# Performance work log

Measured on AMD Instinct MI355X. Metric: run time of the kernel, lower is better.

Reference implementation:

```python
import jax, jax.numpy as jnp
import numpy as np

DIM = 768
HEADS = 12
HEAD_DIM = DIM // HEADS
EPS = 1e-5


def setup_inputs() -> dict:
    key = jax.random.key(0)
    ks = jax.random.split(key, 9)
    s = 0.02
    x = jax.random.normal(ks[0], (4, 1024, DIM), dtype=jnp.float32)
    return {
        "x": x,
        "Wqkv_c": jax.random.normal(ks[1], (DIM, 3 * DIM), jnp.float32) * s,
        "bqkv_c": jnp.zeros((3 * DIM,), jnp.float32),
        "Wp_c": jax.random.normal(ks[2], (DIM, DIM), jnp.float32) * s,
        "bp_c": jnp.zeros((DIM,), jnp.float32),
        "Wqkv_ac": jax.random.normal(ks[3], (DIM, 3 * DIM), jnp.float32) * s,
        "bqkv_ac": jnp.zeros((3 * DIM,), jnp.float32),
        "Wp_ac": jax.random.normal(ks[4], (DIM, DIM), jnp.float32) * s,
        "bp_ac": jnp.zeros((DIM,), jnp.float32),
        "gamma": jnp.ones((DIM,), jnp.float32),
        "beta": jnp.zeros((DIM,), jnp.float32),
    }


def _branch(x, Wqkv, bqkv, Wp, bp, causal: bool):
    B, T, C = x.shape
    qkv = (x @ Wqkv + bqkv).reshape(B, T, 3, HEADS, HEAD_DIM)
    qkv = jnp.transpose(qkv, (2, 0, 3, 1, 4))  # [3,B,H,T,Dh]
    q, k, v = qkv[0], qkv[1], qkv[2]
    scores = jnp.einsum("bhqd,bhkd->bhqk", q, k) / np.sqrt(HEAD_DIM).astype(np.float32)
    i = jnp.arange(T)[:, None]
    j = jnp.arange(T)[None, :]
    mask = (j <= i) if causal else (j >= i)  # tril / triu (incl. diagonal)
    scores = jnp.where(mask[None, None], scores, -jnp.inf)
    attn = jax.nn.softmax(scores, axis=-1)
    out = jnp.einsum("bhqk,bhkd->bhqd", attn, v)
    out = jnp.transpose(out, (0, 2, 1, 3)).reshape(B, T, C)
    return out @ Wp + bp


def reference(x, Wqkv_c, bqkv_c, Wp_c, bp_c, Wqkv_ac, bqkv_ac, Wp_ac, bp_ac, gamma, beta):
    out_c = _branch(x, Wqkv_c, bqkv_c, Wp_c, bp_c, causal=True)
    out_ac = _branch(x, Wqkv_ac, bqkv_ac, Wp_ac, bp_ac, causal=False)
    y = x + out_c + out_ac  # residual; dropout is identity at eval
    mu = jnp.mean(y, axis=-1, keepdims=True)
    var = jnp.var(y, axis=-1, keepdims=True)
    return (y - mu) * jax.lax.rsqrt(var + EPS) * gamma + beta
```

## Files before the change

### kernel.cpp

```cpp
#include <hip/hip_runtime.h>
#include <stdint.h>

#define DIM 768
#define HEADS 12
#define HD 64
#define BATCH 4
#define SEQ 1024
#define NTOK (BATCH*SEQ)
#define QKVW (3*DIM)
#define QKW (2*DIM)
#define EPS 1e-5f

typedef __attribute__((ext_vector_type(8))) short short8;
typedef __attribute__((ext_vector_type(4))) float f32x4;

__device__ __forceinline__ unsigned short f2bf(float f) {
    union { float f; unsigned u; } v; v.f = f;
    unsigned r = v.u + 0x7fffu + ((v.u >> 16) & 1u);
    return (unsigned short)(r >> 16);
}

__device__ __forceinline__ void gld_lds16(const void* g, void* l) {
    auto gp = reinterpret_cast<const __attribute__((address_space(1))) unsigned int*>(
        (uintptr_t)g);
    auto lp = reinterpret_cast<__attribute__((address_space(3))) unsigned int*>(
        (unsigned int)(uintptr_t)l);
    __builtin_amdgcn_global_load_lds(gp, lp, 16, 0, 0);
}

__global__ __launch_bounds__(256) void cvt_kernel(
    const float* __restrict__ in, unsigned short* __restrict__ out)
{
    const int i = blockIdx.x * 256 + threadIdx.x;
    const float4 v = ((const float4*)in)[i];
    ushort4 o4;
    o4.x = f2bf(v.x); o4.y = f2bf(v.y); o4.z = f2bf(v.z); o4.w = f2bf(v.w);
    ((ushort4*)out)[i] = o4;
}

__global__ __launch_bounds__(256) void cvtT_kernel(
    const float* __restrict__ W0, const float* __restrict__ W1,
    unsigned short* __restrict__ T0, unsigned short* __restrict__ T1,
    const int K, const int N)
{
    const float* __restrict__ W = blockIdx.z ? W1 : W0;
    unsigned short* __restrict__ WT = blockIdx.z ? T1 : T0;
    __shared__ float t[32][33];
    const int n0 = blockIdx.x * 32, k0 = blockIdx.y * 32;
    const int c = threadIdx.x & 31, rr = threadIdx.x >> 5;
#pragma unroll
    for (int i = 0; i < 4; ++i)
        t[rr + 8 * i][c] = W[(size_t)(k0 + rr + 8 * i) * N + n0 + c];
    __syncthreads();
#pragma unroll
    for (int i = 0; i < 4; ++i)
        WT[(size_t)(n0 + rr + 8 * i) * K + k0 + c] = f2bf(t[c][rr + 8 * i]);
}

__global__ __launch_bounds__(256) void gemm_qkv_kernel(
    const unsigned short* __restrict__ A,
    const unsigned short* __restrict__ BT0, const unsigned short* __restrict__ BT1,
    const float* __restrict__ bias0, const float* __restrict__ bias1,
    unsigned short* __restrict__ QK0, unsigned short* __restrict__ QK1,
    unsigned short* __restrict__ VT0, unsigned short* __restrict__ VT1)
{
    const int z = blockIdx.z;
    const unsigned short* __restrict__ BT = z ? BT1 : BT0;
    const float* __restrict__ bias = z ? bias1 : bias0;
    unsigned short* __restrict__ QK = z ? QK1 : QK0;
    unsigned short* __restrict__ VT = z ? VT1 : VT0;
    const int K = DIM;

    __shared__ __align__(16) unsigned short Als[2][128 * 32];
    __shared__ __align__(16) unsigned short Bls[2][128 * 32];
    const int tid = threadIdx.x, lane = tid & 63, wv = tid >> 6;
    const int m0 = blockIdx.y * 128, n0 = blockIdx.x * 128;
    const int wr = wv >> 1, wc = wv & 1;
    const int fm = lane & 15, fk = (lane >> 4) * 8;
    const int c0 = wv * 2;
    const int arow = c0 * 16 + (lane >> 2), kk = (lane & 3) * 8;

    const unsigned short* Ag0 = A  + (size_t)(m0 + arow)      * K + kk;
    const unsigned short* Ag1 = A  + (size_t)(m0 + arow + 16) * K + kk;
    const unsigned short* Bg0 = BT + (size_t)(n0 + arow)      * K + kk;
    const unsigned short* Bg1 = BT + (size_t)(n0 + arow + 16) * K + kk;

    f32x4 acc[4][4];
#pragma unroll
    for (int i = 0; i < 4; ++i)
#pragma unroll
        for (int j = 0; j < 4; ++j) acc[i][j] = f32x4{0.f, 0.f, 0.f, 0.f};

    gld_lds16(Ag0, &Als[0][c0 * 512]);
    gld_lds16(Ag1, &Als[0][c0 * 512 + 512]);
    gld_lds16(Bg0, &Bls[0][c0 * 512]);
    gld_lds16(Bg1, &Bls[0][c0 * 512 + 512]);

    const int NK = K / 32;
    for (int kt = 0; kt < NK; ++kt) {
        const int p = kt & 1;
        __syncthreads();
        if (kt + 1 < NK) {
            const int off = (kt + 1) * 32;
            gld_lds16(Ag0 + off, &Als[p ^ 1][c0 * 512]);
            gld_lds16(Ag1 + off, &Als[p ^ 1][c0 * 512 + 512]);
            gld_lds16(Bg0 + off, &Bls[p ^ 1][c0 * 512]);
            gld_lds16(Bg1 + off, &Bls[p ^ 1][c0 * 512 + 512]);
        }
        short8 af[4], bf[4];
#pragma unroll
        for (int i = 0; i < 4; ++i)
            af[i] = *(const short8*)&Als[p][(wr * 64 + i * 16 + fm) * 32 + fk];
#pragma unroll
        for (int j = 0; j < 4; ++j)
            bf[j] = *(const short8*)&Bls[p][(wc * 64 + j * 16 + fm) * 32 + fk];
#pragma unroll
        for (int i = 0; i < 4; ++i)
#pragma unroll
            for (int j = 0; j < 4; ++j)
                acc[i][j] = __builtin_amdgcn_mfma_f32_16x16x32_bf16(af[i], bf[j], acc[i][j], 0, 0, 0);
    }
    const int rbase = (lane >> 4) * 4;
    if (n0 < QKW) {
        const float qsc = (n0 < DIM) ? 0.125f : 1.0f;
#pragma unroll
        for (int i = 0; i < 4; ++i) {
            const int m = m0 + wr * 64 + i * 16 + rbase;
#pragma unroll
            for (int j = 0; j < 4; ++j) {
                const int n = n0 + wc * 64 + j * 16 + fm;
                const float bs = bias[n];
#pragma unroll
                for (int r = 0; r < 4; ++r)
                    QK[(size_t)(m + r) * QKW + n] = f2bf((acc[i][j][r] + bs) * qsc);
            }
        }
    } else {
#pragma unroll
        for (int i = 0; i < 4; ++i) {
            const int m = m0 + wr * 64 + i * 16 + rbase;
            const int b = m >> 10, t = m & 1023;
#pragma unroll
            for (int j = 0; j < 4; ++j) {
                const int n = n0 + wc * 64 + j * 16 + fm;
                const int nh = n - QKW;
                const float bs = bias[n];
                const unsigned p0 = f2bf(acc[i][j][0] + bs);
                const unsigned p1 = f2bf(acc[i][j][1] + bs);
                const unsigned p2 = f2bf(acc[i][j][2] + bs);
                const unsigned p3 = f2bf(acc[i][j][3] + bs);
                uint2 u; u.x = p0 | (p1 << 16); u.y = p2 | (p3 << 16);
                *(uint2*)(VT + ((size_t)((b * HEADS + (nh >> 6)) * HD + (nh & 63)) * SEQ + t)) = u;
            }
        }
    }
}

__global__ __launch_bounds__(256) void gemm_proj_kernel(
    const unsigned short* __restrict__ A0, const unsigned short* __restrict__ BT0,
    const unsigned short* __restrict__ A1, const unsigned short* __restrict__ BT1,
    const float* __restrict__ b0, const float* __restrict__ b1,
    const float* __restrict__ xres, float* __restrict__ Y0, float* __restrict__ Y1)
{
    const int z = blockIdx.z;
    const unsigned short* __restrict__ A  = z ? A1 : A0;
    const unsigned short* __restrict__ BT = z ? BT1 : BT0;
    __shared__ __align__(16) unsigned short Als[2][64 * 32];
    __shared__ __align__(16) unsigned short Bls[2][128 * 32];
    const int tid = threadIdx.x, lane = tid & 63, wv = tid >> 6;
    const int m0 = blockIdx.y * 64, n0 = blockIdx.x * 128;
    const int fm = lane & 15, fg = lane >> 4, fk = (lane >> 4) * 8;
    const int srw = lane >> 2, kk = (lane & 3) * 8;
    const int K = DIM;

    const unsigned short* Ag  = A  + (size_t)(m0 + wv * 16 + srw) * K + kk;
    const unsigned short* Bg0 = BT + (size_t)(n0 + wv * 32 + srw) * K + kk;
    const unsigned short* Bg1 = BT + (size_t)(n0 + wv * 32 + 16 + srw) * K + kk;

    f32x4 acc[4][2];
#pragma unroll
    for (int i = 0; i < 4; ++i)
#pragma unroll
        for (int j = 0; j < 2; ++j) acc[i][j] = f32x4{0.f, 0.f, 0.f, 0.f};

    gld_lds16(Ag,  &Als[0][wv * 512]);
    gld_lds16(Bg0, &Bls[0][wv * 1024]);
    gld_lds16(Bg1, &Bls[0][wv * 1024 + 512]);

    const int NK = K / 32;
    for (int kt = 0; kt < NK; ++kt) {
        const int p = kt & 1;
        __syncthreads();
        if (kt + 1 < NK) {
            const int off = (kt + 1) * 32;
            gld_lds16(Ag + off,  &Als[p ^ 1][wv * 512]);
            gld_lds16(Bg0 + off, &Bls[p ^ 1][wv * 1024]);
            gld_lds16(Bg1 + off, &Bls[p ^ 1][wv * 1024 + 512]);
        }
        short8 af[4], bf[2];
#pragma unroll
        for (int i = 0; i < 4; ++i)
            af[i] = *(const short8*)&Als[p][(i * 16 + fm) * 32 + fk];
#pragma unroll
        for (int j = 0; j < 2; ++j)
            bf[j] = *(const short8*)&Bls[p][(wv * 32 + j * 16 + fm) * 32 + fk];
#pragma unroll
        for (int i = 0; i < 4; ++i)
#pragma unroll
            for (int j = 0; j < 2; ++j)
                acc[i][j] = __builtin_amdgcn_mfma_f32_16x16x32_bf16(af[i], bf[j], acc[i][j], 0, 0, 0);
    }
#pragma unroll
    for (int i = 0; i < 4; ++i) {
        const int m = m0 + i * 16 + fg * 4;
#pragma unroll
        for (int j = 0; j < 2; ++j) {
            const int n = n0 + wv * 32 + j * 16 + fm;
            if (z == 0) {
                const float bs = b0[n] + b1[n];
#pragma unroll
                for (int r = 0; r < 4; ++r) {
                    const size_t idx = (size_t)(m + r) * DIM + n;
                    Y0[idx] = acc[i][j][r] + xres[idx] + bs;
                }
            } else {
#pragma unroll
                for (int r = 0; r < 4; ++r)
                    Y1[(size_t)(m + r) * DIM + n] = acc[i][j][r];
            }
        }
    }
}

#define KP 72
__global__ __launch_bounds__(256, 3) void attn_fused_kernel(
    const unsigned short* __restrict__ qk_c, const unsigned short* __restrict__ vT_c,
    const unsigned short* __restrict__ qk_ac, const unsigned short* __restrict__ vT_ac,
    unsigned short* __restrict__ o_c, unsigned short* __restrict__ o_ac)
{
    __shared__ __align__(16) unsigned short Kls[2][64 * KP];
    __shared__ __align__(16) unsigned short Vls[2][64 * KP];
    __shared__ __align__(16) unsigned short Ps[4][16 * KP];
    const int tid = threadIdx.x, lane = tid & 63, w = tid >> 6;
    const int fm = lane & 15, fg = lane >> 4;
    const int bh = blockIdx.x, qt = blockIdx.y;
    const int b = bh / HEADS, h = bh % HEADS;
    unsigned short* Psw = &Ps[w][0];
    const int srow = tid >> 3, sseg = (tid & 7) * 8;

    for (int br = 0; br < 2; ++br) {
        const int causal = (br == 0);
        const unsigned short* __restrict__ qk = causal ? qk_c : qk_ac;
        const unsigned short* __restrict__ vT = causal ? vT_c : vT_ac;
        unsigned short* __restrict__ o = causal ? o_c : o_ac;
        const unsigned short* qbase = qk + (size_t)b * SEQ * QKW + h * HD;
        const unsigned short* kbase = qbase + DIM;
        const unsigned short* vtb   = vT + (size_t)(b * HEADS + h) * HD * SEQ;

        short8 qb0, qb1;
        {
            const size_t qoff = (size_t)(qt * 64 + w * 16 + fm) * QKW + fg * 8;
            qb0 = *(const short8*)(qbase + qoff);
            qb1 = *(const short8*)(qbase + qoff + 32);
        }

        float ls = 0.f;
        f32x4 accO[4];
#pragma unroll
        for (int dj = 0; dj < 4; ++dj) accO[dj] = f32x4{0.f, 0.f, 0.f, 0.f};

        const int ktb = causal ? 0 : qt;
        const int kte = causal ? qt : (SEQ / 64 - 1);

        uint4 kr0 = *(const uint4*)(kbase + (size_t)(ktb * 64 + srow) * QKW + sseg);
        uint4 kr1 = *(const uint4*)(kbase + (size_t)(ktb * 64 + srow + 32) * QKW + sseg);
        uint4 vr0 = *(const uint4*)(vtb + (size_t)srow * SEQ + ktb * 64 + sseg);
        uint4 vr1 = *(const uint4*)(vtb + (size_t)(srow + 32) * SEQ + ktb * 64 + sseg);

        if (br) __syncthreads();
        int p = 0;
        for (int kt = ktb; kt <= kte; ++kt) {
            *(uint4*)(&Kls[p][srow * KP + sseg])        = kr0;
            *(uint4*)(&Kls[p][(srow + 32) * KP + sseg]) = kr1;
            *(uint4*)(&Vls[p][srow * KP + sseg])        = vr0;
            *(uint4*)(&Vls[p][(srow + 32) * KP + sseg]) = vr1;
            if (kt < kte) {
                const int ktn = kt + 1;
                kr0 = *(const uint4*)(kbase + (size_t)(ktn * 64 + srow) * QKW + sseg);
                kr1 = *(const uint4*)(kbase + (size_t)(ktn * 64 + srow + 32) * QKW + sseg);
                vr0 = *(const uint4*)(vtb + (size_t)srow * SEQ + ktn * 64 + sseg);
                vr1 = *(const uint4*)(vtb + (size_t)(srow + 32) * SEQ + ktn * 64 + sseg);
            }
            __syncthreads();

            f32x4 st[4];
#pragma unroll
            for (int kj = 0; kj < 4; ++kj) {
                const short8 ka0 = *(const short8*)&Kls[p][(kj * 16 + fm) * KP + fg * 8];
                const short8 ka1 = *(const short8*)&Kls[p][(kj * 16 + fm) * KP + 32 + fg * 8];
                st[kj] = __builtin_amdgcn_mfma_f32_16x16x32_bf16(ka0, qb0, f32x4{0.f,0.f,0.f,0.f}, 0, 0, 0);
                st[kj] = __builtin_amdgcn_mfma_f32_16x16x32_bf16(ka1, qb1, st[kj], 0, 0, 0);
            }
            const bool diag = (kt == qt);
#pragma unroll
            for (int kj = 0; kj < 4; ++kj) {
                float e[4];
#pragma unroll
                for (int r = 0; r < 4; ++r) {
                    float v = st[kj][r];
                    if (diag) {
                        const int ki = kj * 16 + fg * 4 + r;
                        const int qi = w * 16 + fm;
                        const bool ok = causal ? (ki <= qi) : (ki >= qi);
                        if (!ok) v = -1e30f;
                    }
                    e[r] = __expf(v);
                    ls += e[r];
                }
                const unsigned p0 = f2bf(e[0]);
                const unsigned p1 = f2bf(e[1]);
                const unsigned p2 = f2bf(e[2]);
                const unsigned p3 = f2bf(e[3]);
                uint2 u; u.x = p0 | (p1 << 16); u.y = p2 | (p3 << 16);
                *(uint2*)(Psw + fm * KP + kj * 16 + fg * 4) = u;
            }
            const short8 ap0 = *(const short8*)(Psw + fm * KP + fg * 8);
            const short8 ap1 = *(const short8*)(Psw + fm * KP + 32 + fg * 8);
#pragma unroll
            for (int dj = 0; dj < 4; ++dj) {
                const short8 vb0 = *(const short8*)&Vls[p][(dj * 16 + fm) * KP + fg * 8];
                const short8 vb1 = *(const short8*)&Vls[p][(dj * 16 + fm) * KP + 32 + fg * 8];
                accO[dj] = __builtin_amdgcn_mfma_f32_16x16x32_bf16(ap0, vb0, accO[dj], 0, 0, 0);
                accO[dj] = __builtin_amdgcn_mfma_f32_16x16x32_bf16(ap1, vb1, accO[dj], 0, 0, 0);
            }
            p ^= 1;
        }

        float lt = ls;
        lt += __shfl_xor(lt, 16);
        lt += __shfl_xor(lt, 32);
        float li_o[4];
#pragma unroll
        for (int r = 0; r < 4; ++r) li_o[r] = __shfl(lt, fg * 4 + r);
#pragma unroll
        for (int r = 0; r < 4; ++r) {
            const float inv = 1.f / li_o[r];
            const int q = qt * 64 + w * 16 + fg * 4 + r;
            unsigned short* orow = o + ((size_t)b * SEQ + q) * DIM + h * HD;
#pragma unroll
            for (int dj = 0; dj < 4; ++dj)
                orow[dj * 16 + fm] = f2bf(accO[dj][r] * inv);
        }
    }
}

__global__ __launch_bounds__(256) void ln_kernel(
    const float* __restrict__ Y0, const float* __restrict__ Y1,
    const float* __restrict__ gamma, const float* __restrict__ beta,
    float* __restrict__ out)
{
    const int row = blockIdx.x;
    const int tid = threadIdx.x;
    const float* y0r = Y0 + (size_t)row * DIM;
    const float* y1r = Y1 + (size_t)row * DIM;
    float v0 = y0r[tid] + y1r[tid];
    float v1 = y0r[tid + 256] + y1r[tid + 256];
    float v2 = y0r[tid + 512] + y1r[tid + 512];
    float s = v0 + v1 + v2;
    float q = v0 * v0 + v1 * v1 + v2 * v2;
#pragma unroll
    for (int off = 32; off > 0; off >>= 1) {
        s += __shfl_down(s, off);
        q += __shfl_down(q, off);
    }
    __shared__ float rs_[4], rq_[4];
    const int wv = tid >> 6;
    if ((tid & 63) == 0) { rs_[wv] = s; rq_[wv] = q; }
    __syncthreads();
    const float ts = rs_[0] + rs_[1] + rs_[2] + rs_[3];
    const float tq = rq_[0] + rq_[1] + rq_[2] + rq_[3];
    const float mu = ts * (1.f / DIM);
    const float var = tq * (1.f / DIM) - mu * mu;
    const float rstd = rsqrtf(var + EPS);
    out[(size_t)row * DIM + tid]       = (v0 - mu) * rstd * gamma[tid]       + beta[tid];
    out[(size_t)row * DIM + tid + 256] = (v1 - mu) * rstd * gamma[tid + 256] + beta[tid + 256];
    out[(size_t)row * DIM + tid + 512] = (v2 - mu) * rstd * gamma[tid + 512] + beta[tid + 512];
}

extern "C" void kernel_launch(void* const* d_in, const int* in_sizes, int n_in,
                              void* d_out, int out_size, void* d_ws, size_t ws_size,
                              hipStream_t stream)
{
    const float* x       = (const float*)d_in[0];
    const float* Wqkv_c  = (const float*)d_in[1];
    const float* bqkv_c  = (const float*)d_in[2];
    const float* Wp_c    = (const float*)d_in[3];
    const float* bp_c    = (const float*)d_in[4];
    const float* Wqkv_ac = (const float*)d_in[5];
    const float* bqkv_ac = (const float*)d_in[6];
    const float* Wp_ac   = (const float*)d_in[7];
    const float* bp_ac   = (const float*)d_in[8];
    const float* gamma   = (const float*)d_in[9];
    const float* beta    = (const float*)d_in[10];
    float* out = (float*)d_out;

    char* p = (char*)d_ws;
    unsigned short* qk_c   = (unsigned short*)p; p += (size_t)NTOK * QKW * 2;
    unsigned short* qk_ac  = (unsigned short*)p; p += (size_t)NTOK * QKW * 2;
    unsigned short* vT_c   = (unsigned short*)p; p += (size_t)NTOK * DIM * 2;
    unsigned short* vT_ac  = (unsigned short*)p; p += (size_t)NTOK * DIM * 2;
    unsigned short* o_ac   = (unsigned short*)p; p += (size_t)NTOK * DIM * 2;
    unsigned short* xb     = (unsigned short*)p; p += (size_t)NTOK * DIM * 2;
    unsigned short* WqT_c  = (unsigned short*)p; p += (size_t)QKVW * DIM * 2;
    unsigned short* WqT_ac = (unsigned short*)p; p += (size_t)QKVW * DIM * 2;
    unsigned short* WpT_c  = (unsigned short*)p; p += (size_t)DIM * DIM * 2;
    unsigned short* WpT_ac = (unsigned short*)p; p += (size_t)DIM * DIM * 2;
    unsigned short* o_c = WqT_c;
    float*          Y0  = (float*)qk_c;
    float*          Y1  = (float*)vT_c;

    cvt_kernel<<<NTOK * DIM / 1024, 256, 0, stream>>>(x, xb);
    cvtT_kernel<<<dim3(QKVW / 32, DIM / 32, 2), 256, 0, stream>>>(
        Wqkv_c, Wqkv_ac, WqT_c, WqT_ac, DIM, QKVW);
    cvtT_kernel<<<dim3(DIM / 32, DIM / 32, 2), 256, 0, stream>>>(
        Wp_c, Wp_ac, WpT_c, WpT_ac, DIM, DIM);

    gemm_qkv_kernel<<<dim3(QKVW / 128, NTOK / 128, 2), 256, 0, stream>>>(
        xb, WqT_c, WqT_ac, bqkv_c, bqkv_ac, qk_c, qk_ac, vT_c, vT_ac);

    attn_fused_kernel<<<dim3(BATCH * HEADS, SEQ / 64), 256, 0, stream>>>(
        qk_c, vT_c, qk_ac, vT_ac, o_c, o_ac);

    gemm_proj_kernel<<<dim3(DIM / 128, NTOK / 64, 2), 256, 0, stream>>>(
        o_c, WpT_c, o_ac, WpT_ac, bp_c, bp_ac, x, Y0, Y1);
    ln_kernel<<<NTOK, 256, 0, stream>>>(Y0, Y1, gamma, beta, out);
}
```

Before: 205.1 us.

## Merge conversion kernels, stage QKV epilogue through LDS, store second projection in bf16

The three input and weight conversion kernels are merged into a single launch that picks its work from the block index. The QKV GEMM epilogue now stages results in a padded shared buffer and writes them out with coalesced 16-byte stores, for both the QK rows and the transposed V. The second projection output is stored as bf16 instead of fp32 to cut write and read traffic into the layernorm. That last step rounds one branch's projection output to bf16 before the residual sum and layernorm, which costs some precision.

Result: faster. 199.9 us (-2.5%).

```diff
diff --git a/kernel.cpp b/kernel.cpp
--- a/kernel.cpp
+++ b/kernel.cpp
@@ -19,6 +19,9 @@
     unsigned r = v.u + 0x7fffu + ((v.u >> 16) & 1u);
     return (unsigned short)(r >> 16);
 }
+__device__ __forceinline__ float b2f(unsigned short s) {
+    union { unsigned u; float f; } v; v.u = (unsigned)s << 16; return v.f;
+}
 
 __device__ __forceinline__ void gld_lds16(const void* g, void* l) {
     auto gp = reinterpret_cast<const __attribute__((address_space(1))) unsigned int*>(
@@ -28,26 +31,40 @@
     __builtin_amdgcn_global_load_lds(gp, lp, 16, 0, 0);
 }
 
-__global__ __launch_bounds__(256) void cvt_kernel(
-    const float* __restrict__ in, unsigned short* __restrict__ out)
-{
-    const int i = blockIdx.x * 256 + threadIdx.x;
-    const float4 v = ((const float4*)in)[i];
-    ushort4 o4;
-    o4.x = f2bf(v.x); o4.y = f2bf(v.y); o4.z = f2bf(v.z); o4.w = f2bf(v.w);
-    ((ushort4*)out)[i] = o4;
-}
-
-__global__ __launch_bounds__(256) void cvtT_kernel(
-    const float* __restrict__ W0, const float* __restrict__ W1,
-    unsigned short* __restrict__ T0, unsigned short* __restrict__ T1,
-    const int K, const int N)
-{
-    const float* __restrict__ W = blockIdx.z ? W1 : W0;
-    unsigned short* __restrict__ WT = blockIdx.z ? T1 : T0;
+#define CVT_X_BLOCKS (NTOK*DIM/1024)
+#define CVT_WQ_TILES ((QKVW/32)*(DIM/32))
+#define CVT_WP_TILES ((DIM/32)*(DIM/32))
+__global__ __launch_bounds__(256) void cvt_all_kernel(
+    const float* __restrict__ x,
+    const float* __restrict__ Wq0, const float* __restrict__ Wq1,
+    const float* __restrict__ Wp0, const float* __restrict__ Wp1,
+    unsigned short* __restrict__ xb,
+    unsigned short* __restrict__ WqT0, unsigned short* __restrict__ WqT1,
+    unsigned short* __restrict__ WpT0, unsigned short* __restrict__ WpT1)
+{
+    const int bid = blockIdx.x, tid = threadIdx.x;
+    if (bid < CVT_X_BLOCKS) {
+        const int i = bid * 256 + tid;
+        const float4 v = ((const float4*)x)[i];
+        ushort4 o4;
+        o4.x = f2bf(v.x); o4.y = f2bf(v.y); o4.z = f2bf(v.z); o4.w = f2bf(v.w);
+        ((ushort4*)xb)[i] = o4;
+        return;
+    }
     __shared__ float t[32][33];
-    const int n0 = blockIdx.x * 32, k0 = blockIdx.y * 32;
-    const int c = threadIdx.x & 31, rr = threadIdx.x >> 5;
+    const float* W; unsigned short* WT; int N, K, tile;
+    int w = bid - CVT_X_BLOCKS;
+    if (w < 2 * CVT_WQ_TILES) {
+        const int z = w / CVT_WQ_TILES; tile = w % CVT_WQ_TILES;
+        W = z ? Wq1 : Wq0; WT = z ? WqT1 : WqT0; N = QKVW; K = DIM;
+    } else {
+        w -= 2 * CVT_WQ_TILES;
+        const int z = w / CVT_WP_TILES; tile = w % CVT_WP_TILES;
+        W = z ? Wp1 : Wp0; WT = z ? WpT1 : WpT0; N = DIM; K = DIM;
+    }
+    const int ntiles = N / 32;
+    const int n0 = (tile % ntiles) * 32, k0 = (tile / ntiles) * 32;
+    const int c = tid & 31, rr = tid >> 5;
 #pragma unroll
     for (int i = 0; i < 4; ++i)
         t[rr + 8 * i][c] = W[(size_t)(k0 + rr + 8 * i) * N + n0 + c];
@@ -71,8 +88,7 @@
     unsigned short* __restrict__ VT = z ? VT1 : VT0;
     const int K = DIM;
 
-    __shared__ __align__(16) unsigned short Als[2][128 * 32];
-    __shared__ __align__(16) unsigned short Bls[2][128 * 32];
+    __shared__ __align__(16) unsigned short sh[17408];
     const int tid = threadIdx.x, lane = tid & 63, wv = tid >> 6;
     const int m0 = blockIdx.y * 128, n0 = blockIdx.x * 128;
     const int wr = wv >> 1, wc = wv & 1;
@@ -91,10 +107,10 @@
 #pragma unroll
         for (int j = 0; j < 4; ++j) acc[i][j] = f32x4{0.f, 0.f, 0.f, 0.f};
 
-    gld_lds16(Ag0, &Als[0][c0 * 512]);
-    gld_lds16(Ag1, &Als[0][c0 * 512 + 512]);
-    gld_lds16(Bg0, &Bls[0][c0 * 512]);
-    gld_lds16(Bg1, &Bls[0][c0 * 512 + 512]);
+    gld_lds16(Ag0, &sh[c0 * 512]);
+    gld_lds16(Ag1, &sh[c0 * 512 + 512]);
+    gld_lds16(Bg0, &sh[4096 + c0 * 512]);
+    gld_lds16(Bg1, &sh[4096 + c0 * 512 + 512]);
 
     const int NK = K / 32;
     for (int kt = 0; kt < NK; ++kt) {
@@ -102,56 +118,76 @@
         __syncthreads();
         if (kt + 1 < NK) {
             const int off = (kt + 1) * 32;
-            gld_lds16(Ag0 + off, &Als[p ^ 1][c0 * 512]);
-            gld_lds16(Ag1 + off, &Als[p ^ 1][c0 * 512 + 512]);
-            gld_lds16(Bg0 + off, &Bls[p ^ 1][c0 * 512]);
-            gld_lds16(Bg1 + off, &Bls[p ^ 1][c0 * 512 + 512]);
-        }
+            const int q = (p ^ 1) * 8192;
+            gld_lds16(Ag0 + off, &sh[q + c0 * 512]);
+            gld_lds16(Ag1 + off, &sh[q + c0 * 512 + 512]);
+            gld_lds16(Bg0 + off, &sh[q + 4096 + c0 * 512]);
+            gld_lds16(Bg1 + off, &sh[q + 4096 + c0 * 512 + 512]);
+        }
+        const int pb = p * 8192;
         short8 af[4], bf[4];
 #pragma unroll
         for (int i = 0; i < 4; ++i)
-            af[i] = *(const short8*)&Als[p][(wr * 64 + i * 16 + fm) * 32 + fk];
+            af[i] = *(const short8*)&sh[pb + (wr * 64 + i * 16 + fm) * 32 + fk];
 #pragma unroll
         for (int j = 0; j < 4; ++j)
-            bf[j] = *(const short8*)&Bls[p][(wc * 64 + j * 16 + fm) * 32 + fk];
+            bf[j] = *(const short8*)&sh[pb + 4096 + (wc * 64 + j * 16 + fm) * 32 + fk];
 #pragma unroll
         for (int i = 0; i < 4; ++i)
 #pragma unroll
             for (int j = 0; j < 4; ++j)
                 acc[i][j] = __builtin_amdgcn_mfma_f32_16x16x32_bf16(af[i], bf[j], acc[i][j], 0, 0, 0);
     }
+
+    __syncthreads();
     const int rbase = (lane >> 4) * 4;
+    const int rowg = tid >> 4, lseg = tid & 15;
     if (n0 < QKW) {
         const float qsc = (n0 < DIM) ? 0.125f : 1.0f;
 #pragma unroll
         for (int i = 0; i < 4; ++i) {
-            const int m = m0 + wr * 64 + i * 16 + rbase;
+            const int ml = wr * 64 + i * 16 + rbase;
 #pragma unroll
             for (int j = 0; j < 4; ++j) {
-                const int n = n0 + wc * 64 + j * 16 + fm;
-                const float bs = bias[n];
+                const int nl = wc * 64 + j * 16 + fm;
+                const float bs = bias[n0 + nl];
 #pragma unroll
                 for (int r = 0; r < 4; ++r)
-                    QK[(size_t)(m + r) * QKW + n] = f2bf((acc[i][j][r] + bs) * qsc);
-            }
+                    sh[(ml + r) * 136 + nl] = f2bf((acc[i][j][r] + bs) * qsc);
+            }
+        }
+        __syncthreads();
+#pragma unroll
+        for (int pp = 0; pp < 8; ++pp) {
+            const int row = pp * 16 + rowg;
+            const uint4 v = *(const uint4*)&sh[row * 136 + lseg * 8];
+            *(uint4*)(QK + (size_t)(m0 + row) * QKW + n0 + lseg * 8) = v;
         }
     } else {
+        const int b = m0 >> 10, t0 = m0 & 1023;
 #pragma unroll
         for (int i = 0; i < 4; ++i) {
-            const int m = m0 + wr * 64 + i * 16 + rbase;
-            const int b = m >> 10, t = m & 1023;
+            const int tl = wr * 64 + i * 16 + rbase;
 #pragma unroll
             for (int j = 0; j < 4; ++j) {
-                const int n = n0 + wc * 64 + j * 16 + fm;
-                const int nh = n - QKW;
-                const float bs = bias[n];
+                const int nl = wc * 64 + j * 16 + fm;
+                const float bs = bias[n0 + nl];
                 const unsigned p0 = f2bf(acc[i][j][0] + bs);
                 const unsigned p1 = f2bf(acc[i][j][1] + bs);
                 const unsigned p2 = f2bf(acc[i][j][2] + bs);
                 const unsigned p3 = f2bf(acc[i][j][3] + bs);
                 uint2 u; u.x = p0 | (p1 << 16); u.y = p2 | (p3 << 16);
-                *(uint2*)(VT + ((size_t)((b * HEADS + (nh >> 6)) * HD + (nh & 63)) * SEQ + t)) = u;
-            }
+                *(uint2*)(&sh[nl * 136 + tl]) = u;
+            }
+        }
+        __syncthreads();
+#pragma unroll
+        for (int pp = 0; pp < 8; ++pp) {
+            const int nl = pp * 16 + rowg;
+            const int nh = (n0 - QKW) + nl;
+            const uint4 v = *(const uint4*)&sh[nl * 136 + lseg * 8];
+            *(uint4*)(VT + ((size_t)((b * HEADS + (nh >> 6)) * HD + (nh & 63))) * SEQ
+                      + t0 + lseg * 8) = v;
         }
     }
 }
@@ -160,7 +196,8 @@
     const unsigned short* __restrict__ A0, const unsigned short* __restrict__ BT0,
     const unsigned short* __restrict__ A1, const unsigned short* __restrict__ BT1,
     const float* __restrict__ b0, const float* __restrict__ b1,
-    const float* __restrict__ xres, float* __restrict__ Y0, float* __restrict__ Y1)
+    const float* __restrict__ xres, float* __restrict__ Y0,
+    unsigned short* __restrict__ Y1)
 {
     const int z = blockIdx.z;
     const unsigned short* __restrict__ A  = z ? A1 : A0;
@@ -226,7 +263,7 @@
             } else {
 #pragma unroll
                 for (int r = 0; r < 4; ++r)
-                    Y1[(size_t)(m + r) * DIM + n] = acc[i][j][r];
+                    Y1[(size_t)(m + r) * DIM + n] = f2bf(acc[i][j][r]);
             }
         }
     }
@@ -355,17 +392,17 @@
 }
 
 __global__ __launch_bounds__(256) void ln_kernel(
-    const float* __restrict__ Y0, const float* __restrict__ Y1,
+    const float* __restrict__ Y0, const unsigned short* __restrict__ Y1,
     const float* __restrict__ gamma, const float* __restrict__ beta,
     float* __restrict__ out)
 {
     const int row = blockIdx.x;
     const int tid = threadIdx.x;
     const float* y0r = Y0 + (size_t)row * DIM;
-    const float* y1r = Y1 + (size_t)row * DIM;
-    float v0 = y0r[tid] + y1r[tid];
-    float v1 = y0r[tid + 256] + y1r[tid + 256];
-    float v2 = y0r[tid + 512] + y1r[tid + 512];
+    const unsigned short* y1r = Y1 + (size_t)row * DIM;
+    float v0 = y0r[tid]       + b2f(y1r[tid]);
+    float v1 = y0r[tid + 256] + b2f(y1r[tid + 256]);
+    float v2 = y0r[tid + 512] + b2f(y1r[tid + 512]);
     float s = v0 + v1 + v2;
     float q = v0 * v0 + v1 * v1 + v2 * v2;
 #pragma unroll
@@ -417,13 +454,10 @@
     unsigned short* WpT_ac = (unsigned short*)p; p += (size_t)DIM * DIM * 2;
     unsigned short* o_c = WqT_c;
     float*          Y0  = (float*)qk_c;
-    float*          Y1  = (float*)vT_c;
-
-    cvt_kernel<<<NTOK * DIM / 1024, 256, 0, stream>>>(x, xb);
-    cvtT_kernel<<<dim3(QKVW / 32, DIM / 32, 2), 256, 0, stream>>>(
-        Wqkv_c, Wqkv_ac, WqT_c, WqT_ac, DIM, QKVW);
-    cvtT_kernel<<<dim3(DIM / 32, DIM / 32, 2), 256, 0, stream>>>(
-        Wp_c, Wp_ac, WpT_c, WpT_ac, DIM, DIM);
+    unsigned short* Y1  = vT_c;
+
+    cvt_all_kernel<<<CVT_X_BLOCKS + 2 * CVT_WQ_TILES + 2 * CVT_WP_TILES, 256, 0, stream>>>(
+        x, Wqkv_c, Wqkv_ac, Wp_c, Wp_ac, xb, WqT_c, WqT_ac, WpT_c, WpT_ac);
 
     gemm_qkv_kernel<<<dim3(QKVW / 128, NTOK / 128, 2), 256, 0, stream>>>(
         xb, WqT_c, WqT_ac, bqkv_c, bqkv_ac, qk_c, qk_ac, vT_c, vT_ac);
```
